# Kernel optimization log

Measured on AMD Instinct MI355X. Metric: run time of the kernel, lower is better.

Reference implementation:

```python
import jax, jax.numpy as jnp
import numpy as np

B, C, T = 8, 1024, 1500          # batch, WavLM feature dim, frames
K = 8192                         # linguistic centroid bank size
D, H = 256, 512                  # refiner embed dim, MLP hidden dim
NQ, BINS = 4, 1024               # RVQ stages, codebook bins per stage
LRELU_SLOPE = 0.01               # torch LeakyReLU default
EPS = 1e-8


def setup_inputs():
    key = jax.random.key(0)
    ks = jax.random.split(key, 24)
    w = lambda k, s: jax.random.normal(k, s, dtype=jnp.float32) * 0.02
    inp = {
        'feature': jax.random.normal(ks[0], (B, C, T), dtype=jnp.float32),
        'centroid': jax.random.normal(ks[1], (K, C), dtype=jnp.float32),
        # SpeakerRefiner encoder: 1024->512->512->256 (LeakyReLU between)
        'enc_w0': w(ks[2], (C, H)), 'enc_b0': w(ks[3], (H,)),
        'enc_w1': w(ks[4], (H, H)), 'enc_b1': w(ks[5], (H,)),
        'enc_w2': w(ks[6], (H, D)), 'enc_b2': w(ks[7], (D,)),
        # SpeakerRefiner decoder: 256->512->512->1024 (LeakyReLU between)
        'dec_w0': w(ks[8], (D, H)), 'dec_b0': w(ks[9], (H,)),
        'dec_w1': w(ks[10], (H, H)), 'dec_b1': w(ks[11], (H,)),
        'dec_w2': w(ks[12], (H, C)), 'dec_b2': w(ks[13], (C,)),
        # SpeakerNormalizer: 1024->512->512->256, ReLU after EVERY layer
        'nrm_w0': w(ks[14], (C, H)), 'nrm_b0': w(ks[15], (H,)),
        'nrm_w1': w(ks[16], (H, H)), 'nrm_b1': w(ks[17], (H,)),
        'nrm_w2': w(ks[18], (H, D)), 'nrm_b2': w(ks[19], (D,)),
        # RVQ codebooks, one per stage
        'codebooks': jax.random.normal(ks[20], (NQ, BINS, D), dtype=jnp.float32),
    }
    return inp


def _nn_gather(x_flat, table):
    """argmin of squared distances (x^2 - 2 x.C^T + C^2) + row gather."""
    dist = ((x_flat ** 2).sum(1, keepdims=True)
            - 2.0 * x_flat @ table.T
            + (table ** 2).sum(1)[None, :])
    idx = jnp.argmin(dist, axis=1)
    return table[idx]


def reference(feature, centroid,
              enc_w0, enc_b0, enc_w1, enc_b1, enc_w2, enc_b2,
              dec_w0, dec_b0, dec_w1, dec_b1, dec_w2, dec_b2,
              nrm_w0, nrm_b0, nrm_w1, nrm_b1, nrm_w2, nrm_b2,
              codebooks):
    lrelu = lambda v: jax.nn.leaky_relu(v, LRELU_SLOPE)

    def enc(z):  # (B,T,C) -> (B,T,D)
        h0 = lrelu(z @ enc_w0 + enc_b0)
        h1 = lrelu(h0 @ enc_w1 + enc_b1)
        return h1 @ enc_w2 + enc_b2

    def dec(z):  # (B,T,D) -> (B,T,C)
        h0 = lrelu(z @ dec_w0 + dec_b0)
        h1 = lrelu(h0 @ dec_w1 + dec_b1)
        return h1 @ dec_w2 + dec_b2

    def nrm(z):  # (B,T,C) -> (B,T,D), ReLU after each Linear
        h0 = jax.nn.relu(z @ nrm_w0 + nrm_b0)
        h1 = jax.nn.relu(h0 @ nrm_w1 + nrm_b1)
        return jax.nn.relu(h1 @ nrm_w2 + nrm_b2)

    # ---- linguistic VQ: cdist + argmin + gather over centroid bank ----
    x_flat = feature.transpose(0, 2, 1).reshape(-1, C)        # (B*T, C)
    lin_dec_bt = _nn_gather(x_flat, centroid).reshape(B, T, C)  # (B,T,C)
    lin_dec = lin_dec_bt.transpose(0, 2, 1)                    # (B,C,T)

    # ---- speaker residual path ----
    spk_raw = feature - lin_dec                                # (B,C,T)
    spk_enc = enc(spk_raw.transpose(0, 2, 1))                  # (B,T,D)
    norm_vec = nrm(lin_dec_bt)                                 # (B,T,D)  (iteration > norm_start_step branch)
    spk_enc_norm = spk_enc / (norm_vec + EPS)

    # ---- residual vector quantizer (n_q stages, straight-through) ----
    residual, q_sum = spk_enc_norm, jnp.zeros_like(spk_enc_norm)
    for i in range(NQ):
        q = _nn_gather(residual.reshape(-1, D), codebooks[i]).reshape(B, T, D)
        q_sum = q_sum + q
        residual = residual - q
    quantized = spk_enc_norm + jax.lax.stop_gradient(q_sum - spk_enc_norm)

    # ---- denorm + decode + combine ----
    spk_enc_denorm = quantized * norm_vec
    spk_dec = dec(spk_enc_denorm).transpose(0, 2, 1)           # (B,C,T)
    dec_feature = lin_dec + spk_dec                            # quantize == [1,1]
    return dec_feature
```

## Files before the change

### kernel.cpp

```cpp
#include <hip/hip_runtime.h>

namespace {

constexpr int kB = 8;
constexpr int kC = 1024;
constexpr int kT = 1500;
constexpr int kK = 8192;
constexpr int kD = 256;
constexpr int kH = 512;
constexpr int kNQ = 4;
constexpr int kBins = 1024;
constexpr int kN = kB * kT;
constexpr float kEps = 1e-8f;
constexpr float kSlope = 0.01f;
constexpr float kMargin = 8.0f;
constexpr unsigned kCap = 4194304;

using u64 = unsigned long long;
typedef __attribute__((ext_vector_type(8))) short bf16x8;
typedef __attribute__((ext_vector_type(4))) float f32x4;

__device__ __forceinline__ unsigned ordered_bits(float f) {
  unsigned b = __float_as_uint(f);
  return (b & 0x80000000u) ? ~b : (b | 0x80000000u);
}
__device__ __forceinline__ float unordered_bits(unsigned b) {
  return __uint_as_float((b & 0x80000000u) ? (b ^ 0x80000000u) : ~b);
}
__device__ __forceinline__ unsigned short f2bf(float f) {
  unsigned u = __float_as_uint(f);
  return (unsigned short)((u + 0x7fffu + ((u >> 16) & 1u)) >> 16);
}
__device__ __forceinline__ void gl_lds16(const void* g, void* l) {
  __builtin_amdgcn_global_load_lds(
      (const __attribute__((address_space(1))) void*)g,
      (__attribute__((address_space(3))) void*)l, 16, 0, 0);
}

__device__ __forceinline__ void stage_tile(const unsigned short* __restrict__ g,
                                           int rowlen, int r0, int k0,
                                           unsigned short* lds,
                                           int w, int srow, int sp) {
#pragma unroll
  for (int i = 0; i < 2; ++i) {
    const int rb = (w * 2 + i) * 16;
    const int r = rb + srow;
    const int s = (sp - ((r >> 1) & 3)) & 3;
    gl_lds16(g + ((size_t)(r0 + r) * rowlen + k0 + s * 8), lds + rb * 32);
  }
}

__global__ __launch_bounds__(256) void transpose_in(const float* __restrict__ f,
                                                    float* __restrict__ X) {
  __shared__ float tile[32][33];
  const int t0 = blockIdx.x * 32, c0 = blockIdx.y * 32, b = blockIdx.z;
  const int tx = threadIdx.x, ty = threadIdx.y;
#pragma unroll
  for (int i = 0; i < 4; ++i) {
    const int cl = ty + i * 8;
    if (t0 + tx < kT)
      tile[cl][tx] = f[(size_t)b * kC * kT + (size_t)(c0 + cl) * kT + (t0 + tx)];
  }
  __syncthreads();
#pragma unroll
  for (int i = 0; i < 4; ++i) {
    const int tl = ty + i * 8;
    if (t0 + tl < kT)
      X[(size_t)(b * kT + t0 + tl) * kC + (c0 + tx)] = tile[tx][tl];
  }
}

__global__ __launch_bounds__(256) void to_bf16(const float* __restrict__ in,
                                               unsigned short* __restrict__ out,
                                               int n4) {
  const int i = blockIdx.x * 256 + threadIdx.x;
  if (i >= n4) return;
  const float4 v = reinterpret_cast<const float4*>(in)[i];
  ushort4 o;
  o.x = f2bf(v.x); o.y = f2bf(v.y); o.z = f2bf(v.z); o.w = f2bf(v.w);
  reinterpret_cast<ushort4*>(out)[i] = o;
}

__global__ __launch_bounds__(256) void transpose_w_bf16(
    const float* __restrict__ W, unsigned short* __restrict__ WT, int K, int N) {
  __shared__ float tile[32][33];
  const int k0 = blockIdx.x * 32, n0 = blockIdx.y * 32;
  const int tx = threadIdx.x, ty = threadIdx.y;
#pragma unroll
  for (int i = 0; i < 4; ++i)
    tile[ty + i * 8][tx] = W[(size_t)(k0 + ty + i * 8) * N + (n0 + tx)];
  __syncthreads();
#pragma unroll
  for (int i = 0; i < 4; ++i)
    WT[(size_t)(n0 + ty + i * 8) * K + (k0 + tx)] = f2bf(tile[tx][ty + i * 8]);
}

__global__ __launch_bounds__(256) void row_sqsum(const float* __restrict__ A,
                                                 float* __restrict__ S, int Kd) {
  const int r = blockIdx.x;
  const float4* a4 = reinterpret_cast<const float4*>(A + (size_t)r * Kd);
  float s = 0.f;
  for (int i = threadIdx.x; i < (Kd >> 2); i += 256) {
    const float4 v = a4[i];
    s = fmaf(v.x, v.x, s); s = fmaf(v.y, v.y, s);
    s = fmaf(v.z, v.z, s); s = fmaf(v.w, v.w, s);
  }
#pragma unroll
  for (int off = 32; off > 0; off >>= 1) s += __shfl_down(s, off, 64);
  __shared__ float ws[4];
  const int lane = threadIdx.x & 63, w = threadIdx.x >> 6;
  if (lane == 0) ws[w] = s;
  __syncthreads();
  if (threadIdx.x == 0) S[r] = (ws[0] + ws[1]) + (ws[2] + ws[3]);
}

__global__ __launch_bounds__(256) void lin_vq_mfma(
    const unsigned short* __restrict__ Ah, const unsigned short* __restrict__ Bh,
    const float* __restrict__ S, const float* __restrict__ cc,
    unsigned* __restrict__ rowmin, unsigned* __restrict__ cands,
    unsigned* __restrict__ counter, int M) {
  __shared__ __attribute__((aligned(16))) unsigned short lsa[2][128 * 32];
  __shared__ __attribute__((aligned(16))) unsigned short lsb[2][128 * 32];
  const int t = threadIdx.x;
  const int l = t & 63, w = t >> 6;
  const int wr = w >> 1, wc = w & 1;
  const int rl = l & 15, lh = l >> 4;
  const int srow = l >> 2, sp = l & 3;
  const unsigned nbx = gridDim.x;
  const unsigned flat = blockIdx.y * nbx + blockIdx.x;
  const unsigned q8 = (nbx * gridDim.y) >> 3;
  const unsigned swz = (flat & 7u) * q8 + (flat >> 3);
  const int m0 = (int)(swz % nbx) * 128, n0 = (int)(swz / nbx) * 128;

  f32x4 acc[4][4] = {};
  stage_tile(Ah, kC, m0, 0, lsa[0], w, srow, sp);
  stage_tile(Bh, kC, n0, 0, lsb[0], w, srow, sp);
  __syncthreads();
  for (int kt = 0; kt < kC / 32; ++kt) {
    const int p = kt & 1;
    if (kt + 1 < kC / 32) {
      stage_tile(Ah, kC, m0, (kt + 1) * 32, lsa[p ^ 1], w, srow, sp);
      stage_tile(Bh, kC, n0, (kt + 1) * 32, lsb[p ^ 1], w, srow, sp);
    }
    bf16x8 a[4], b[4];
#pragma unroll
    for (int m = 0; m < 4; ++m) {
      const int r = wr * 64 + m * 16 + rl;
      const int pp = (lh + ((r >> 1) & 3)) & 3;
      a[m] = *reinterpret_cast<const bf16x8*>(&lsa[p][r * 32 + pp * 8]);
    }
#pragma unroll
    for (int n = 0; n < 4; ++n) {
      const int r = wc * 64 + n * 16 + rl;
      const int pp = (lh + ((r >> 1) & 3)) & 3;
      b[n] = *reinterpret_cast<const bf16x8*>(&lsb[p][r * 32 + pp * 8]);
    }
#pragma unroll
    for (int m = 0; m < 4; ++m)
#pragma unroll
      for (int n = 0; n < 4; ++n)
        acc[m][n] = __builtin_amdgcn_mfma_f32_16x16x32_bf16(a[m], b[n], acc[m][n], 0, 0, 0);
    __syncthreads();
  }
  float ccv[4];
#pragma unroll
  for (int n = 0; n < 4; ++n) ccv[n] = cc[n0 + wc * 64 + n * 16 + rl];
#pragma unroll
  for (int m = 0; m < 4; ++m) {
#pragma unroll
    for (int j = 0; j < 4; ++j) {
      const int gr = m0 + wr * 64 + m * 16 + lh * 4 + j;
      const bool valid = gr < M;
      const float Sv = valid ? S[gr] : 0.f;
      float mn = 3.4e38f;
#pragma unroll
      for (int n = 0; n < 4; ++n) {
        const float d = fmaf(-2.f, acc[m][n][j], Sv) + ccv[n];
        acc[m][n][j] = d;
        mn = fminf(mn, d);
      }
#pragma unroll
      for (int mask = 1; mask < 16; mask <<= 1)
        mn = fminf(mn, __shfl_xor(mn, mask, 64));
      if (valid && rl == 0) atomicMin(&rowmin[gr], ordered_bits(mn));
    }
  }
  __threadfence();
#pragma unroll
  for (int m = 0; m < 4; ++m) {
#pragma unroll
    for (int j = 0; j < 4; ++j) {
      const int gr = m0 + wr * 64 + m * 16 + lh * 4 + j;
      if (gr >= M) continue;
      const float thr = unordered_bits(rowmin[gr]) + kMargin;
#pragma unroll
      for (int n = 0; n < 4; ++n) {
        if (acc[m][n][j] <= thr) {
          const unsigned gc = (unsigned)(n0 + wc * 64 + n * 16 + rl);
          const unsigned slot = atomicAdd(counter, 1u);
          if (slot < kCap) cands[slot] = (unsigned)gr * 8192u + gc;
        }
      }
    }
  }
}

template <int ACT, int OUTBF>
__global__ __launch_bounds__(256) void gemm_bf16(
    const unsigned short* __restrict__ A, const unsigned short* __restrict__ WT,
    const float* __restrict__ bias, void* __restrict__ outp,
    int M, int N, int K) {
  __shared__ __attribute__((aligned(16))) unsigned short lsa[2][128 * 32];
  __shared__ __attribute__((aligned(16))) unsigned short lsb[2][128 * 32];
  const int t = threadIdx.x;
  const int l = t & 63, w = t >> 6;
  const int wr = w >> 1, wc = w & 1;
  const int rl = l & 15, lh = l >> 4;
  const int srow = l >> 2, sp = l & 3;
  const unsigned nbx = gridDim.x;
  const unsigned nwg = nbx * gridDim.y;
  const unsigned flat = blockIdx.y * nbx + blockIdx.x;
  unsigned swz = flat;
  if ((nwg & 7u) == 0) swz = (flat & 7u) * (nwg >> 3) + (flat >> 3);
  const int m0 = (int)(swz % nbx) * 128, n0 = (int)(swz / nbx) * 128;

  f32x4 acc[4][4] = {};
  stage_tile(A, K, m0, 0, lsa[0], w, srow, sp);
  stage_tile(WT, K, n0, 0, lsb[0], w, srow, sp);
  __syncthreads();
  const int NT = K >> 5;
  for (int kt = 0; kt < NT; ++kt) {
    const int p = kt & 1;
    if (kt + 1 < NT) {
      stage_tile(A, K, m0, (kt + 1) * 32, lsa[p ^ 1], w, srow, sp);
      stage_tile(WT, K, n0, (kt + 1) * 32, lsb[p ^ 1], w, srow, sp);
    }
    bf16x8 a[4], b[4];
#pragma unroll
    for (int m = 0; m < 4; ++m) {
      const int r = wr * 64 + m * 16 + rl;
      const int pp = (lh + ((r >> 1) & 3)) & 3;
      a[m] = *reinterpret_cast<const bf16x8*>(&lsa[p][r * 32 + pp * 8]);
    }
#pragma unroll
    for (int n = 0; n < 4; ++n) {
      const int r = wc * 64 + n * 16 + rl;
      const int pp = (lh + ((r >> 1) & 3)) & 3;
      b[n] = *reinterpret_cast<const bf16x8*>(&lsb[p][r * 32 + pp * 8]);
    }
#pragma unroll
    for (int m = 0; m < 4; ++m)
#pragma unroll
      for (int n = 0; n < 4; ++n)
        acc[m][n] = __builtin_amdgcn_mfma_f32_16x16x32_bf16(a[m], b[n], acc[m][n], 0, 0, 0);
    __syncthreads();
  }
  float bv[4];
#pragma unroll
  for (int n = 0; n < 4; ++n) bv[n] = bias[n0 + wc * 64 + n * 16 + rl];
#pragma unroll
  for (int m = 0; m < 4; ++m) {
#pragma unroll
    for (int j = 0; j < 4; ++j) {
      const int gr = m0 + wr * 64 + m * 16 + lh * 4 + j;
      if (gr >= M) continue;
#pragma unroll
      for (int n = 0; n < 4; ++n) {
        float v = acc[m][n][j] + bv[n];
        if (ACT == 1) v = (v >= 0.f) ? v : kSlope * v;
        const int gc = n0 + wc * 64 + n * 16 + rl;
        if (OUTBF) ((unsigned short*)outp)[(size_t)gr * N + gc] = f2bf(v);
        else       ((float*)outp)[(size_t)gr * N + gc] = v;
      }
    }
  }
}

__global__ __launch_bounds__(256) void rescore(
    const float* __restrict__ X, const float* __restrict__ Cn,
    const float* __restrict__ S, const float* __restrict__ cc,
    const unsigned* __restrict__ cands, const unsigned* __restrict__ counter,
    u64* __restrict__ keys) {
  const unsigned nc = min(*counter, kCap);
  const int l = threadIdx.x & 63;
  const unsigned wglob = (blockIdx.x * 256 + threadIdx.x) >> 6;
  const unsigned nw = (gridDim.x * 256) >> 6;
  for (unsigned i = wglob; i < nc; i += nw) {
    const unsigned pc = cands[i];
    const int r = pc >> 13, c = pc & 8191;
    const float4* xr = reinterpret_cast<const float4*>(X + (size_t)r * kC);
    const float4* cr = reinterpret_cast<const float4*>(Cn + (size_t)c * kC);
    float acc = 0.f;
#pragma unroll
    for (int q = 0; q < 4; ++q) {
      const float4 a = xr[l * 4 + q], b = cr[l * 4 + q];
      acc = fmaf(a.x, b.x, acc); acc = fmaf(a.y, b.y, acc);
      acc = fmaf(a.z, b.z, acc); acc = fmaf(a.w, b.w, acc);
    }
#pragma unroll
    for (int off = 32; off > 0; off >>= 1) acc += __shfl_down(acc, off, 64);
    if (l == 0) {
      const float d = (S[r] - 2.0f * acc) + cc[c];
      atomicMin(&keys[r], ((u64)ordered_bits(d) << 32) | (unsigned)c);
    }
  }
}

__global__ __launch_bounds__(256) void vq_argmin(
    const float* __restrict__ A, const float* __restrict__ table,
    const float* __restrict__ cc, const float* __restrict__ S,
    u64* __restrict__ keys, int M, int Kd) {
  __shared__ float As[16][128];
  __shared__ float Ts[16][128];
  __shared__ u64 red[128][16];
  const int m0 = blockIdx.x * 128, n0 = blockIdx.y * 128;
  const int t = threadIdx.x;
  const int tx = t & 15, ty = t >> 4;
  const int lrow = t >> 1, lk8 = (t & 1) * 8;
  float acc[8][8] = {};
  for (int k0 = 0; k0 < Kd; k0 += 16) {
    const int gm = m0 + lrow;
    float4 a0 = make_float4(0.f, 0.f, 0.f, 0.f), a1 = a0;
    if (gm < M) {
      const float* ap = &A[(size_t)gm * Kd + (k0 + lk8)];
      a0 = *reinterpret_cast<const float4*>(ap);
      a1 = *reinterpret_cast<const float4*>(ap + 4);
    }
    const float* tp = &table[(size_t)(n0 + lrow) * Kd + (k0 + lk8)];
    const float4 b0 = *reinterpret_cast<const float4*>(tp);
    const float4 b1 = *reinterpret_cast<const float4*>(tp + 4);
    As[lk8 + 0][lrow] = a0.x; As[lk8 + 1][lrow] = a0.y;
    As[lk8 + 2][lrow] = a0.z; As[lk8 + 3][lrow] = a0.w;
    As[lk8 + 4][lrow] = a1.x; As[lk8 + 5][lrow] = a1.y;
    As[lk8 + 6][lrow] = a1.z; As[lk8 + 7][lrow] = a1.w;
    Ts[lk8 + 0][lrow] = b0.x; Ts[lk8 + 1][lrow] = b0.y;
    Ts[lk8 + 2][lrow] = b0.z; Ts[lk8 + 3][lrow] = b0.w;
    Ts[lk8 + 4][lrow] = b1.x; Ts[lk8 + 5][lrow] = b1.y;
    Ts[lk8 + 6][lrow] = b1.z; Ts[lk8 + 7][lrow] = b1.w;
    __syncthreads();
#pragma unroll
    for (int kk = 0; kk < 16; ++kk) {
      float ar[8], br[8];
      *reinterpret_cast<float4*>(&ar[0]) = *reinterpret_cast<const float4*>(&As[kk][ty * 8]);
      *reinterpret_cast<float4*>(&ar[4]) = *reinterpret_cast<const float4*>(&As[kk][ty * 8 + 4]);
      *reinterpret_cast<float4*>(&br[0]) = *reinterpret_cast<const float4*>(&Ts[kk][tx * 8]);
      *reinterpret_cast<float4*>(&br[4]) = *reinterpret_cast<const float4*>(&Ts[kk][tx * 8 + 4]);
#pragma unroll
      for (int i = 0; i < 8; ++i)
#pragma unroll
        for (int j = 0; j < 8; ++j) acc[i][j] = fmaf(ar[i], br[j], acc[i][j]);
    }
    __syncthreads();
  }
  float ccv[8];
  *reinterpret_cast<float4*>(&ccv[0]) = *reinterpret_cast<const float4*>(&cc[n0 + tx * 8]);
  *reinterpret_cast<float4*>(&ccv[4]) = *reinterpret_cast<const float4*>(&cc[n0 + tx * 8 + 4]);
#pragma unroll
  for (int i = 0; i < 8; ++i) {
    const int gm = m0 + ty * 8 + i;
    const float Srow = (gm < M) ? S[gm] : 0.f;
    u64 best = ~0ull;
#pragma unroll
    for (int j = 0; j < 8; ++j) {
      const int gn = n0 + tx * 8 + j;
      const float d = (Srow - 2.0f * acc[i][j]) + ccv[j];
      const u64 key = ((u64)ordered_bits(d) << 32) | (unsigned)gn;
      best = (key < best) ? key : best;
    }
    red[ty * 8 + i][tx] = best;
  }
  __syncthreads();
  if (t < 128) {
    u64 b = red[t][0];
#pragma unroll
    for (int j = 1; j < 16; ++j) { const u64 v = red[t][j]; b = (v < b) ? v : b; }
    const int gm = m0 + t;
    if (gm < M) atomicMin(&keys[gm], b);
  }
}

__global__ __launch_bounds__(256) void gather_residual(
    const float* __restrict__ centroid, const u64* __restrict__ keys,
    float* __restrict__ X, float* __restrict__ lin_dec) {
  const int i4 = blockIdx.x * 256 + threadIdx.x;
  const int n = i4 >> 8;
  const int c4 = (i4 & 255) << 2;
  const unsigned idx = (unsigned)(keys[n] & 0xffffffffu);
  const float4 cv = *reinterpret_cast<const float4*>(&centroid[(size_t)idx * kC + c4]);
  float4 xv = *reinterpret_cast<const float4*>(&X[(size_t)n * kC + c4]);
  xv.x -= cv.x; xv.y -= cv.y; xv.z -= cv.z; xv.w -= cv.w;
  *reinterpret_cast<float4*>(&lin_dec[(size_t)n * kC + c4]) = cv;
  *reinterpret_cast<float4*>(&X[(size_t)n * kC + c4]) = xv;
}

template <int ACT>
__global__ __launch_bounds__(256) void gemm_bias_act(
    const float* __restrict__ A, const float* __restrict__ W,
    const float* __restrict__ bias, float* __restrict__ out,
    int M, int Nc, int Kd) {
  __shared__ float As[16][64];
  __shared__ float Ws[16][64];
  const int m0 = blockIdx.x * 64, n0 = blockIdx.y * 64;
  const int t = threadIdx.x;
  const int tx = t & 15, ty = t >> 4;
  const int arow = t >> 2, ak4 = (t & 3) << 2;
  const int wk = t >> 4, wn4 = (t & 15) << 2;
  float acc[4][4] = {};
  for (int k0 = 0; k0 < Kd; k0 += 16) {
    float4 av = make_float4(0.f, 0.f, 0.f, 0.f);
    const int gm = m0 + arow;
    if (gm < M) av = *reinterpret_cast<const float4*>(&A[(size_t)gm * Kd + (k0 + ak4)]);
    As[ak4 + 0][arow] = av.x; As[ak4 + 1][arow] = av.y;
    As[ak4 + 2][arow] = av.z; As[ak4 + 3][arow] = av.w;
    *reinterpret_cast<float4*>(&Ws[wk][wn4]) =
        *reinterpret_cast<const float4*>(&W[(size_t)(k0 + wk) * Nc + (n0 + wn4)]);
    __syncthreads();
#pragma unroll
    for (int kk = 0; kk < 16; ++kk) {
      float ar[4], br[4];
      *reinterpret_cast<float4*>(ar) = *reinterpret_cast<const float4*>(&As[kk][ty << 2]);
      *reinterpret_cast<float4*>(br) = *reinterpret_cast<const float4*>(&Ws[kk][tx << 2]);
#pragma unroll
      for (int i = 0; i < 4; ++i)
#pragma unroll
        for (int j = 0; j < 4; ++j) acc[i][j] = fmaf(ar[i], br[j], acc[i][j]);
    }
    __syncthreads();
  }
  float bv[4];
  *reinterpret_cast<float4*>(bv) = *reinterpret_cast<const float4*>(&bias[n0 + (tx << 2)]);
#pragma unroll
  for (int i = 0; i < 4; ++i) {
    const int gm = m0 + (ty << 2) + i;
    if (gm >= M) continue;
    float o[4];
#pragma unroll
    for (int j = 0; j < 4; ++j) {
      float v = acc[i][j] + bv[j];
      if (ACT == 1) v = (v >= 0.f) ? v : kSlope * v;
      if (ACT == 2) v = fmaxf(v, 0.f);
      o[j] = v;
    }
    *reinterpret_cast<float4*>(&out[(size_t)gm * Nc + n0 + (tx << 2)]) =
        *reinterpret_cast<const float4*>(o);
  }
}

__global__ __launch_bounds__(256) void norm_div_init(
    const float* __restrict__ e, const float* __restrict__ nv,
    float* __restrict__ resid, float* __restrict__ qsum) {
  const int i = blockIdx.x * 256 + threadIdx.x;
  const float4 ev = reinterpret_cast<const float4*>(e)[i];
  const float4 vv = reinterpret_cast<const float4*>(nv)[i];
  float4 r;
  r.x = ev.x / (vv.x + kEps); r.y = ev.y / (vv.y + kEps);
  r.z = ev.z / (vv.z + kEps); r.w = ev.w / (vv.w + kEps);
  reinterpret_cast<float4*>(resid)[i] = r;
  reinterpret_cast<float4*>(qsum)[i] = make_float4(0.f, 0.f, 0.f, 0.f);
}

__global__ __launch_bounds__(256) void rvq_update(
    const float* __restrict__ cb, const u64* __restrict__ keys,
    float* __restrict__ resid, float* __restrict__ qsum) {
  const int i4 = blockIdx.x * 256 + threadIdx.x;
  const int n = i4 >> 6;
  const int d4 = (i4 & 63) << 2;
  const unsigned idx = (unsigned)(keys[n] & 0xffffffffu);
  const float4 q = *reinterpret_cast<const float4*>(&cb[(size_t)idx * kD + d4]);
  float4 r = reinterpret_cast<float4*>(resid)[i4];
  float4 s = reinterpret_cast<float4*>(qsum)[i4];
  r.x -= q.x; r.y -= q.y; r.z -= q.z; r.w -= q.w;
  s.x += q.x; s.y += q.y; s.z += q.z; s.w += q.w;
  reinterpret_cast<float4*>(resid)[i4] = r;
  reinterpret_cast<float4*>(qsum)[i4] = s;
}

__global__ __launch_bounds__(256) void denorm_bf16(
    const float* __restrict__ qsum, const float* __restrict__ nv,
    unsigned short* __restrict__ o) {
  const int i = blockIdx.x * 256 + threadIdx.x;
  const float4 q = reinterpret_cast<const float4*>(qsum)[i];
  const float4 v = reinterpret_cast<const float4*>(nv)[i];
  ushort4 r;
  r.x = f2bf(q.x * v.x); r.y = f2bf(q.y * v.y);
  r.z = f2bf(q.z * v.z); r.w = f2bf(q.w * v.w);
  reinterpret_cast<ushort4*>(o)[i] = r;
}

__global__ __launch_bounds__(256) void final_out(const float* __restrict__ lin_dec,
                                                 const float* __restrict__ dec_out,
                                                 float* __restrict__ out) {
  __shared__ float tile[32][33];
  const int t0 = blockIdx.x * 32, c0 = blockIdx.y * 32, b = blockIdx.z;
  const int tx = threadIdx.x, ty = threadIdx.y;
#pragma unroll
  for (int i = 0; i < 4; ++i) {
    const int tl = ty + i * 8;
    if (t0 + tl < kT) {
      const size_t idx = (size_t)(b * kT + t0 + tl) * kC + (c0 + tx);
      tile[tl][tx] = lin_dec[idx] + dec_out[idx];
    }
  }
  __syncthreads();
#pragma unroll
  for (int i = 0; i < 4; ++i) {
    const int cl = ty + i * 8;
    if (t0 + tx < kT)
      out[(size_t)b * kC * kT + (size_t)(c0 + cl) * kT + (t0 + tx)] = tile[tx][cl];
  }
}

}

extern "C" void kernel_launch(void* const* d_in, const int* in_sizes, int n_in,
                              void* d_out, int out_size, void* d_ws, size_t ws_size,
                              hipStream_t stream) {
  (void)in_sizes; (void)n_in; (void)out_size; (void)ws_size;
  const float* feature  = (const float*)d_in[0];
  const float* centroid = (const float*)d_in[1];
  const float* enc_w0 = (const float*)d_in[2];  const float* enc_b0 = (const float*)d_in[3];
  const float* enc_w1 = (const float*)d_in[4];  const float* enc_b1 = (const float*)d_in[5];
  const float* enc_w2 = (const float*)d_in[6];  const float* enc_b2 = (const float*)d_in[7];
  const float* dec_w0 = (const float*)d_in[8];  const float* dec_b0 = (const float*)d_in[9];
  const float* dec_w1 = (const float*)d_in[10]; const float* dec_b1 = (const float*)d_in[11];
  const float* dec_w2 = (const float*)d_in[12]; const float* dec_b2 = (const float*)d_in[13];
  const float* nrm_w0 = (const float*)d_in[14]; const float* nrm_b0 = (const float*)d_in[15];
  const float* nrm_w1 = (const float*)d_in[16]; const float* nrm_b1 = (const float*)d_in[17];
  const float* nrm_w2 = (const float*)d_in[18]; const float* nrm_b2 = (const float*)d_in[19];
  const float* codebooks = (const float*)d_in[20];
  float* out = (float*)d_out;

  float* X       = (float*)d_ws;
  float* lin_dec = X       + (size_t)kN * kC;
  float* h0      = lin_dec + (size_t)kN * kC;
  float* h1      = h0      + (size_t)kN * kH;
  float* e_out   = h1      + (size_t)kN * kH;
  float* nvec    = e_out   + (size_t)kN * kD;
  float* resid   = nvec    + (size_t)kN * kD;
  float* qsum    = resid   + (size_t)kN * kD;
  float* Srow    = qsum    + (size_t)kN * kD;
  float* ccbuf   = Srow    + kN;
  u64*   keys    = (u64*)(ccbuf + kK);

  unsigned short* xh = (unsigned short*)h0;
  unsigned short* ch = (unsigned short*)h1;
  unsigned* cands    = (unsigned*)lin_dec;
  unsigned* rowmin   = (unsigned*)(h1 + 4500000);
  unsigned* counter  = rowmin + kN;
  unsigned short* dec_in_bf = (unsigned short*)e_out;
  unsigned short* h0b = (unsigned short*)h0;
  unsigned short* h1b = (unsigned short*)h1;
  unsigned short* wT0 = (unsigned short*)(h0 + 3200000);
  unsigned short* wT1 = wT0 + (size_t)kH * kD;
  unsigned short* wT2 = wT1 + (size_t)kH * kH;

  const dim3 tb32(32, 8);
  const dim3 tgT((kT + 31) / 32, kC / 32, kB);

  transpose_in<<<tgT, tb32, 0, stream>>>(feature, X);

  row_sqsum<<<kN, 256, 0, stream>>>(X, Srow, kC);
  row_sqsum<<<kK, 256, 0, stream>>>(centroid, ccbuf, kC);
  to_bf16<<<(kN * kC / 4 + 255) / 256, 256, 0, stream>>>(X, xh, kN * kC / 4);
  to_bf16<<<(kK * kC / 4 + 255) / 256, 256, 0, stream>>>(centroid, ch, kK * kC / 4);
  hipMemsetAsync(rowmin, 0xFF, (size_t)kN * sizeof(unsigned), stream);
  hipMemsetAsync(counter, 0x00, sizeof(unsigned), stream);
  hipMemsetAsync(keys, 0xFF, (size_t)kN * sizeof(u64), stream);
  lin_vq_mfma<<<dim3((kN + 127) / 128, kK / 128), 256, 0, stream>>>(
      xh, ch, Srow, ccbuf, rowmin, cands, counter, kN);
  rescore<<<512, 256, 0, stream>>>(X, centroid, Srow, ccbuf, cands, counter, keys);
  gather_residual<<<kN * kC / 4 / 256, 256, 0, stream>>>(centroid, keys, X, lin_dec);

  const dim3 gH((kN + 63) / 64, kH / 64);
  const dim3 gD((kN + 63) / 64, kD / 64);

  gemm_bias_act<1><<<gH, 256, 0, stream>>>(X,  enc_w0, enc_b0, h0,    kN, kH, kC);
  gemm_bias_act<1><<<gH, 256, 0, stream>>>(h0, enc_w1, enc_b1, h1,    kN, kH, kH);
  gemm_bias_act<0><<<gD, 256, 0, stream>>>(h1, enc_w2, enc_b2, e_out, kN, kD, kH);

  gemm_bias_act<2><<<gH, 256, 0, stream>>>(lin_dec, nrm_w0, nrm_b0, h0,   kN, kH, kC);
  gemm_bias_act<2><<<gH, 256, 0, stream>>>(h0,      nrm_w1, nrm_b1, h1,   kN, kH, kH);
  gemm_bias_act<2><<<gD, 256, 0, stream>>>(h1,      nrm_w2, nrm_b2, nvec, kN, kD, kH);

  norm_div_init<<<kN * kD / 4 / 256, 256, 0, stream>>>(e_out, nvec, resid, qsum);

  for (int q = 0; q < kNQ; ++q) {
    const float* cb = codebooks + (size_t)q * kBins * kD;
    row_sqsum<<<kN, 256, 0, stream>>>(resid, Srow, kD);
    row_sqsum<<<kBins, 256, 0, stream>>>(cb, ccbuf, kD);
    hipMemsetAsync(keys, 0xFF, (size_t)kN * sizeof(u64), stream);
    vq_argmin<<<dim3((kN + 127) / 128, kBins / 128), 256, 0, stream>>>(
        resid, cb, ccbuf, Srow, keys, kN, kD);
    rvq_update<<<kN * kD / 4 / 256, 256, 0, stream>>>(cb, keys, resid, qsum);
  }

  transpose_w_bf16<<<dim3(kD / 32, kH / 32), tb32, 0, stream>>>(dec_w0, wT0, kD, kH);
  transpose_w_bf16<<<dim3(kH / 32, kH / 32), tb32, 0, stream>>>(dec_w1, wT1, kH, kH);
  transpose_w_bf16<<<dim3(kH / 32, kC / 32), tb32, 0, stream>>>(dec_w2, wT2, kH, kC);
  denorm_bf16<<<kN * kD / 4 / 256, 256, 0, stream>>>(qsum, nvec, dec_in_bf);
  gemm_bf16<1, 1><<<dim3((kN + 127) / 128, kH / 128), 256, 0, stream>>>(
      dec_in_bf, wT0, dec_b0, h0b, kN, kH, kD);
  gemm_bf16<1, 1><<<dim3((kN + 127) / 128, kH / 128), 256, 0, stream>>>(
      h0b, wT1, dec_b1, h1b, kN, kH, kH);
  gemm_bf16<0, 0><<<dim3((kN + 127) / 128, kC / 128), 256, 0, stream>>>(
      h1b, wT2, dec_b2, X, kN, kC, kH);

  final_out<<<tgT, tb32, 0, stream>>>(lin_dec, X, out);
}
```

Measured before the change: 2.469 ms.

## Enlarge fp32 MLP GEMM tiles to 128x128 and retune block scheduling

The fp32 encoder and normalizer GEMMs move from 64x64 tiles with 4x4 per-thread outputs to 128x128 tiles with 8x8 per-thread outputs. This raises arithmetic intensity per shared-memory load and halves global traffic per FLOP, at the cost of more registers and possibly lower occupancy. The centroid-distance MFMA kernel gets a new block-to-tile mapping that groups M-tiles into three row bands with eight N-tiles per group, aimed at L2 reuse. The bf16 GEMM drops its swizzle in favour of plain linear ordering.

```diff
diff --git a/kernel.cpp b/kernel.cpp
--- a/kernel.cpp
+++ b/kernel.cpp
@@ -126,11 +126,16 @@
   const int wr = w >> 1, wc = w & 1;
   const int rl = l & 15, lh = l >> 4;
   const int srow = l >> 2, sp = l & 3;
-  const unsigned nbx = gridDim.x;
-  const unsigned flat = blockIdx.y * nbx + blockIdx.x;
-  const unsigned q8 = (nbx * gridDim.y) >> 3;
-  const unsigned swz = (flat & 7u) * q8 + (flat >> 3);
-  const int m0 = (int)(swz % nbx) * 128, n0 = (int)(swz / nbx) * 128;
+  const unsigned flat = blockIdx.y * gridDim.x + blockIdx.x;
+  unsigned r, rem;
+  if (flat < 4096u) { r = flat >> 11; rem = flat & 2047u; }
+  else { r = 2u; rem = flat - 4096u; }
+  const unsigned h = (r < 2u) ? 32u : 30u;
+  const unsigned g = rem / (h * 8u);
+  const unsigned wv = rem % (h * 8u);
+  const unsigned mi = wv % h, ni = wv / h;
+  const int m0 = (int)(r * 32u + mi) * 128;
+  const int n0 = (int)(g * 8u + ni) * 128;
 
   f32x4 acc[4][4] = {};
   stage_tile(Ah, kC, m0, 0, lsa[0], w, srow, sp);
@@ -145,15 +150,15 @@
     bf16x8 a[4], b[4];
 #pragma unroll
     for (int m = 0; m < 4; ++m) {
-      const int r = wr * 64 + m * 16 + rl;
-      const int pp = (lh + ((r >> 1) & 3)) & 3;
-      a[m] = *reinterpret_cast<const bf16x8*>(&lsa[p][r * 32 + pp * 8]);
+      const int rr = wr * 64 + m * 16 + rl;
+      const int pp = (lh + ((rr >> 1) & 3)) & 3;
+      a[m] = *reinterpret_cast<const bf16x8*>(&lsa[p][rr * 32 + pp * 8]);
     }
 #pragma unroll
     for (int n = 0; n < 4; ++n) {
-      const int r = wc * 64 + n * 16 + rl;
-      const int pp = (lh + ((r >> 1) & 3)) & 3;
-      b[n] = *reinterpret_cast<const bf16x8*>(&lsb[p][r * 32 + pp * 8]);
+      const int rr = wc * 64 + n * 16 + rl;
+      const int pp = (lh + ((rr >> 1) & 3)) & 3;
+      b[n] = *reinterpret_cast<const bf16x8*>(&lsb[p][rr * 32 + pp * 8]);
     }
 #pragma unroll
     for (int m = 0; m < 4; ++m)
@@ -218,11 +223,8 @@
   const int rl = l & 15, lh = l >> 4;
   const int srow = l >> 2, sp = l & 3;
   const unsigned nbx = gridDim.x;
-  const unsigned nwg = nbx * gridDim.y;
   const unsigned flat = blockIdx.y * nbx + blockIdx.x;
-  unsigned swz = flat;
-  if ((nwg & 7u) == 0) swz = (flat & 7u) * (nwg >> 3) + (flat >> 3);
-  const int m0 = (int)(swz % nbx) * 128, n0 = (int)(swz / nbx) * 128;
+  const int m0 = (int)(flat % nbx) * 128, n0 = (int)(flat / nbx) * 128;
 
   f32x4 acc[4][4] = {};
   stage_tile(A, K, m0, 0, lsa[0], w, srow, sp);
@@ -238,15 +240,15 @@
     bf16x8 a[4], b[4];
 #pragma unroll
     for (int m = 0; m < 4; ++m) {
-      const int r = wr * 64 + m * 16 + rl;
-      const int pp = (lh + ((r >> 1) & 3)) & 3;
-      a[m] = *reinterpret_cast<const bf16x8*>(&lsa[p][r * 32 + pp * 8]);
+      const int rr = wr * 64 + m * 16 + rl;
+      const int pp = (lh + ((rr >> 1) & 3)) & 3;
+      a[m] = *reinterpret_cast<const bf16x8*>(&lsa[p][rr * 32 + pp * 8]);
     }
 #pragma unroll
     for (int n = 0; n < 4; ++n) {
-      const int r = wc * 64 + n * 16 + rl;
-      const int pp = (lh + ((r >> 1) & 3)) & 3;
-      b[n] = *reinterpret_cast<const bf16x8*>(&lsb[p][r * 32 + pp * 8]);
+      const int rr = wc * 64 + n * 16 + rl;
+      const int pp = (lh + ((rr >> 1) & 3)) & 3;
+      b[n] = *reinterpret_cast<const bf16x8*>(&lsb[p][rr * 32 + pp * 8]);
     }
 #pragma unroll
     for (int m = 0; m < 4; ++m)
@@ -394,55 +396,66 @@
 }
 
 template <int ACT>
-__global__ __launch_bounds__(256) void gemm_bias_act(
+__global__ __launch_bounds__(256) void gemm_f32_128(
     const float* __restrict__ A, const float* __restrict__ W,
     const float* __restrict__ bias, float* __restrict__ out,
     int M, int Nc, int Kd) {
-  __shared__ float As[16][64];
-  __shared__ float Ws[16][64];
-  const int m0 = blockIdx.x * 64, n0 = blockIdx.y * 64;
+  __shared__ float As[16][128];
+  __shared__ float Ws[16][128];
+  const int m0 = blockIdx.x * 128, n0 = blockIdx.y * 128;
   const int t = threadIdx.x;
   const int tx = t & 15, ty = t >> 4;
-  const int arow = t >> 2, ak4 = (t & 3) << 2;
-  const int wk = t >> 4, wn4 = (t & 15) << 2;
-  float acc[4][4] = {};
+  const int lrow = t >> 1, lk8 = (t & 1) * 8;
+  const int wk = t >> 4, wn8 = (t & 15) * 8;
+  float acc[8][8] = {};
   for (int k0 = 0; k0 < Kd; k0 += 16) {
-    float4 av = make_float4(0.f, 0.f, 0.f, 0.f);
-    const int gm = m0 + arow;
-    if (gm < M) av = *reinterpret_cast<const float4*>(&A[(size_t)gm * Kd + (k0 + ak4)]);
-    As[ak4 + 0][arow] = av.x; As[ak4 + 1][arow] = av.y;
-    As[ak4 + 2][arow] = av.z; As[ak4 + 3][arow] = av.w;
-    *reinterpret_cast<float4*>(&Ws[wk][wn4]) =
-        *reinterpret_cast<const float4*>(&W[(size_t)(k0 + wk) * Nc + (n0 + wn4)]);
+    const int gm = m0 + lrow;
+    float4 a0 = make_float4(0.f, 0.f, 0.f, 0.f), a1 = a0;
+    if (gm < M) {
+      const float* ap = &A[(size_t)gm * Kd + (k0 + lk8)];
+      a0 = *reinterpret_cast<const float4*>(ap);
+      a1 = *reinterpret_cast<const float4*>(ap + 4);
+    }
+    As[lk8 + 0][lrow] = a0.x; As[lk8 + 1][lrow] = a0.y;
+    As[lk8 + 2][lrow] = a0.z; As[lk8 + 3][lrow] = a0.w;
+    As[lk8 + 4][lrow] = a1.x; As[lk8 + 5][lrow] = a1.y;
+    As[lk8 + 6][lrow] = a1.z; As[lk8 + 7][lrow] = a1.w;
+    const float* wp = &W[(size_t)(k0 + wk) * Nc + (n0 + wn8)];
+    *reinterpret_cast<float4*>(&Ws[wk][wn8]) = *reinterpret_cast<const float4*>(wp);
+    *reinterpret_cast<float4*>(&Ws[wk][wn8 + 4]) = *reinterpret_cast<const float4*>(wp + 4);
     __syncthreads();
 #pragma unroll
     for (int kk = 0; kk < 16; ++kk) {
-      float ar[4], br[4];
-      *reinterpret_cast<float4*>(ar) = *reinterpret_cast<const float4*>(&As[kk][ty << 2]);
-      *reinterpret_cast<float4*>(br) = *reinterpret_cast<const float4*>(&Ws[kk][tx << 2]);
-#pragma unroll
-      for (int i = 0; i < 4; ++i)
-#pragma unroll
-        for (int j = 0; j < 4; ++j) acc[i][j] = fmaf(ar[i], br[j], acc[i][j]);
+      float ar[8], br[8];
+      *reinterpret_cast<float4*>(&ar[0]) = *reinterpret_cast<const float4*>(&As[kk][ty * 8]);
+      *reinterpret_cast<float4*>(&ar[4]) = *reinterpret_cast<const float4*>(&As[kk][ty * 8 + 4]);
+      *reinterpret_cast<float4*>(&br[0]) = *reinterpret_cast<const float4*>(&Ws[kk][tx * 8]);
+      *reinterpret_cast<float4*>(&br[4]) = *reinterpret_cast<const float4*>(&Ws[kk][tx * 8 + 4]);
+#pragma unroll
+      for (int i = 0; i < 8; ++i)
+#pragma unroll
+        for (int j = 0; j < 8; ++j) acc[i][j] = fmaf(ar[i], br[j], acc[i][j]);
     }
     __syncthreads();
   }
-  float bv[4];
-  *reinterpret_cast<float4*>(bv) = *reinterpret_cast<const float4*>(&bias[n0 + (tx << 2)]);
-#pragma unroll
-  for (int i = 0; i < 4; ++i) {
-    const int gm = m0 + (ty << 2) + i;
+  float bv[8];
+  *reinterpret_cast<float4*>(&bv[0]) = *reinterpret_cast<const float4*>(&bias[n0 + tx * 8]);
+  *reinterpret_cast<float4*>(&bv[4]) = *reinterpret_cast<const float4*>(&bias[n0 + tx * 8 + 4]);
+#pragma unroll
+  for (int i = 0; i < 8; ++i) {
+    const int gm = m0 + ty * 8 + i;
     if (gm >= M) continue;
-    float o[4];
-#pragma unroll
-    for (int j = 0; j < 4; ++j) {
+    float o[8];
+#pragma unroll
+    for (int j = 0; j < 8; ++j) {
       float v = acc[i][j] + bv[j];
       if (ACT == 1) v = (v >= 0.f) ? v : kSlope * v;
       if (ACT == 2) v = fmaxf(v, 0.f);
       o[j] = v;
     }
-    *reinterpret_cast<float4*>(&out[(size_t)gm * Nc + n0 + (tx << 2)]) =
-        *reinterpret_cast<const float4*>(o);
+    float* op = &out[(size_t)gm * Nc + n0 + tx * 8];
+    *reinterpret_cast<float4*>(op) = *reinterpret_cast<const float4*>(&o[0]);
+    *reinterpret_cast<float4*>(op + 4) = *reinterpret_cast<const float4*>(&o[4]);
   }
 }
 
@@ -571,16 +584,16 @@
   rescore<<<512, 256, 0, stream>>>(X, centroid, Srow, ccbuf, cands, counter, keys);
   gather_residual<<<kN * kC / 4 / 256, 256, 0, stream>>>(centroid, keys, X, lin_dec);
 
-  const dim3 gH((kN + 63) / 64, kH / 64);
-  const dim3 gD((kN + 63) / 64, kD / 64);
-
-  gemm_bias_act<1><<<gH, 256, 0, stream>>>(X,  enc_w0, enc_b0, h0,    kN, kH, kC);
-  gemm_bias_act<1><<<gH, 256, 0, stream>>>(h0, enc_w1, enc_b1, h1,    kN, kH, kH);
-  gemm_bias_act<0><<<gD, 256, 0, stream>>>(h1, enc_w2, enc_b2, e_out, kN, kD, kH);
-
-  gemm_bias_act<2><<<gH, 256, 0, stream>>>(lin_dec, nrm_w0, nrm_b0, h0,   kN, kH, kC);
-  gemm_bias_act<2><<<gH, 256, 0, stream>>>(h0,      nrm_w1, nrm_b1, h1,   kN, kH, kH);
-  gemm_bias_act<2><<<gD, 256, 0, stream>>>(h1,      nrm_w2, nrm_b2, nvec, kN, kD, kH);
+  const dim3 gH128((kN + 127) / 128, kH / 128);
+  const dim3 gD128((kN + 127) / 128, kD / 128);
+
+  gemm_f32_128<1><<<gH128, 256, 0, stream>>>(X,  enc_w0, enc_b0, h0,    kN, kH, kC);
+  gemm_f32_128<1><<<gH128, 256, 0, stream>>>(h0, enc_w1, enc_b1, h1,    kN, kH, kH);
+  gemm_f32_128<0><<<gD128, 256, 0, stream>>>(h1, enc_w2, enc_b2, e_out, kN, kD, kH);
+
+  gemm_f32_128<2><<<gH128, 256, 0, stream>>>(lin_dec, nrm_w0, nrm_b0, h0,   kN, kH, kC);
+  gemm_f32_128<2><<<gH128, 256, 0, stream>>>(h0,      nrm_w1, nrm_b1, h1,   kN, kH, kH);
+  gemm_f32_128<2><<<gD128, 256, 0, stream>>>(h1,      nrm_w2, nrm_b2, nvec, kN, kD, kH);
 
   norm_div_init<<<kN * kD / 4 / 256, 256, 0, stream>>>(e_out, nvec, resid, qsum);
 
```

Result: no change. 2.513 ms (+1.8%).
